# Optimization experiments

Measured on AMD Instinct MI355X. Metric: run time of the kernel, lower is better.

Reference implementation:

```python
import jax, jax.numpy as jnp
import numpy as np

K = 9          # kernel_size
PAD = K // 2   # same padding
SIGMA = 1.0
EPS = 1e-5     # BatchNorm eps


def setup_inputs() -> dict:
    key = jax.random.key(0)
    k0, k1, k2 = jax.random.split(key, 3)
    B, Cin, Cout, L = 4, 64, 64, 131072
    x = jax.random.normal(k0, (B, Cin, L), jnp.float32)
    coords = jax.random.uniform(k1, (B, 3, L), jnp.float32)  # 3D point coords in [0,1)
    W = jax.random.normal(k2, (Cout, Cin, K), jnp.float32) * (1.0 / np.sqrt(Cin * K))
    bias = jnp.zeros((Cout,), jnp.float32)
    gamma = jnp.ones((Cout,), jnp.float32)
    beta = jnp.zeros((Cout,), jnp.float32)
    return {"x": x, "coords": coords, "W": W, "bias": bias, "gamma": gamma, "beta": beta}


def reference(x, coords, W, bias, gamma, beta):
    B, Cin, L = x.shape
    # zero-pad sequence dim for 'same' conv
    xpad = jnp.pad(x, ((0, 0), (0, 0), (PAD, PAD)))
    cpad = jnp.pad(coords, ((0, 0), (0, 0), (PAD, PAD)))
    # unfold: neighbor windows of size K (K is a small compile-time constant)
    x_unf = jnp.stack([xpad[:, :, k:k + L] for k in range(K)], axis=2)   # [B,Cin,K,L]
    c_unf = jnp.stack([cpad[:, :, k:k + L] for k in range(K)], axis=2)   # [B,3,K,L]
    # Gaussian spatial weights from coord distances (WeightedConv1D)
    dist2 = jnp.sum((c_unf - coords[:, :, None, :]) ** 2, axis=1)        # [B,K,L]
    w = jnp.exp(-dist2 / (2.0 * SIGMA * SIGMA))                          # [B,K,L]
    # weighted conv: contract over (Cin, K)
    out = jnp.einsum('ock,bckl->bol', W, x_unf * w[:, None, :, :])       # [B,Cout,L]
    out = out + bias[None, :, None]
    # BatchNorm1d (training-mode batch statistics over B and L) + ReLU
    mean = out.mean(axis=(0, 2), keepdims=True)
    var = out.var(axis=(0, 2), keepdims=True)
    out = (out - mean) * jax.lax.rsqrt(var + EPS)
    out = out * gamma[None, :, None] + beta[None, :, None]
    return jax.nn.relu(out)
```

## Files before the change

kernel.cpp:

```cpp
#include <hip/hip_runtime.h>
#include <hip/hip_bf16.h>

#define KK 9
#define PADK 4
#define CIN 64
#define COUT 64
#define LSEQ 131072
#define NB 4
#define TILEL 128
#define XROWS 136
#define XRS 72
#define NTILES 1024
#define NPART 64
#define TPB 4
#define GRIDC (NB * NTILES / TPB)

typedef __attribute__((ext_vector_type(8))) short v8s;
typedef __attribute__((ext_vector_type(4))) float v4f;

__device__ __forceinline__ unsigned short f2bf(float f) {
  __hip_bfloat16 h = __float2bfloat16(f);
  return *reinterpret_cast<unsigned short*>(&h);
}
__device__ __forceinline__ float bf2f(unsigned short s) {
  return __uint_as_float(((unsigned)s) << 16);
}

__device__ __forceinline__ void store_o(float* p, float v) { *p = v; }
__device__ __forceinline__ void store_o(__hip_bfloat16* p, float v) { *p = __float2bfloat16(v); }

__global__ void wtrans_kernel(const float* __restrict__ W, v8s* __restrict__ Wt) {
  int t = blockIdx.x * 256 + threadIdx.x;
  if (t >= KK * 2 * 4 * 64) return;
  int lane = t & 63;
  int frag = t >> 6;
  int mblk = frag & 3;
  int s    = (frag >> 2) & 1;
  int k    = frag >> 3;
  int m = lane & 15, q = lane >> 4;
  int o = mblk * 16 + m;
  union { v8s v; unsigned short h[8]; } u;
#pragma unroll
  for (int j = 0; j < 8; ++j) {
    int c = 32 * s + q * 8 + j;
    u.h[j] = f2bf(W[(o * CIN + c) * KK + k]);
  }
  Wt[t] = u.v;
}

template <typename OutT>
__global__ __launch_bounds__(256, 3)
void conv_kernel(const float* __restrict__ x, const float* __restrict__ coords,
                 const v8s* __restrict__ Wt, OutT* __restrict__ cv,
                 float* __restrict__ stat_sum, float* __restrict__ stat_sq) {
  __shared__ __align__(16) __hip_bfloat16 xt[2][XROWS][XRS];
  __shared__ float wt[2][KK][TILEL];

  const int tid  = threadIdx.x;
  const int wv   = tid >> 6;
  const int wo   = wv & 1;
  const int wl   = wv >> 1;
  const int lane = tid & 63;
  const int m = lane & 15;
  const int q = lane >> 4;

  const int bid = blockIdx.x;
  const int b   = bid >> 8;
  const int t0  = (bid & 255) * TPB;
  const float* xb = x + (b * CIN) * LSEQ;
  const float* cb = coords + (b * 3) * LSEQ;
  OutT* outb = cv + (b * COUT) * LSEQ;

  const int cg = tid & 7, lc = tid >> 3, c8 = cg * 8;
  const int cn = tid >> 1;
  const int khalf = tid & 1;
  const int k0 = khalf * 4;

  float4 f[8];
  float4 hx;
  float sx, sy, sz;
  float cxk[5], cyk[5], czk[5];

  auto prefetch = [&](int tile) {
    const int l0 = tile * TILEL;
#pragma unroll
    for (int t = 0; t < 8; ++t)
      f[t] = *(const float4*)(xb + (c8 + t) * LSEQ + l0 + 4 * lc);
    if (tid < 128) {
      int side = tid >> 6, c = tid & 63;
      hx = make_float4(0.f, 0.f, 0.f, 0.f);
      if (side == 0) {
        if (tile != 0) hx = *(const float4*)(xb + c * LSEQ + l0 - 4);
      } else {
        if (tile != NTILES - 1) hx = *(const float4*)(xb + c * LSEQ + l0 + TILEL);
      }
    }
    sx = cb[l0 + cn];
    sy = cb[LSEQ + l0 + cn];
    sz = cb[2 * LSEQ + l0 + cn];
#pragma unroll
    for (int i = 0; i < 5; ++i) {
      int l = l0 + cn + (k0 + i) - PADK;
      float cx = 0.f, cy = 0.f, cz = 0.f;
      if ((unsigned)l < (unsigned)LSEQ) {
        cx = cb[l]; cy = cb[LSEQ + l]; cz = cb[2 * LSEQ + l];
      }
      cxk[i] = cx; cyk[i] = cy; czk[i] = cz;
    }
  };

  prefetch(t0);

#pragma unroll 1
  for (int ti = 0; ti < TPB; ++ti) {
    const int tile = t0 + ti;
    const int l0 = tile * TILEL;
    const int cur = ti & 1;

    {
      const float* fp = (const float*)&f[0];
#pragma unroll
      for (int j = 0; j < 4; ++j) {
        union { v8s v; unsigned short h[8]; } u;
#pragma unroll
        for (int t = 0; t < 8; ++t) u.h[t] = f2bf(fp[4 * t + j]);
        *(v8s*)&xt[cur][4 + 4 * lc + j][c8] = u.v;
      }
      if (tid < 128) {
        int side = tid >> 6, c = tid & 63;
        int rb = side ? (TILEL + PADK) : 0;
        xt[cur][rb + 0][c] = __float2bfloat16(hx.x);
        xt[cur][rb + 1][c] = __float2bfloat16(hx.y);
        xt[cur][rb + 2][c] = __float2bfloat16(hx.z);
        xt[cur][rb + 3][c] = __float2bfloat16(hx.w);
      }
      float w5[5];
#pragma unroll
      for (int i = 0; i < 5; ++i) {
        float dx = cxk[i] - sx, dy = cyk[i] - sy, dz = czk[i] - sz;
        w5[i] = __expf(-0.5f * (dx * dx + dy * dy + dz * dz));
      }
      if (khalf == 0) {
#pragma unroll
        for (int i = 0; i < 4; ++i) wt[cur][i][cn] = w5[i] - w5[i + 1];
      } else {
#pragma unroll
        for (int i = 0; i < 4; ++i) wt[cur][4 + i][cn] = w5[i] - w5[i + 1];
        wt[cur][8][cn] = w5[4];
      }
    }

    if (ti + 1 < TPB) prefetch(tile + 1);

    asm volatile("s_waitcnt lgkmcnt(0)" ::: "memory");
    __builtin_amdgcn_s_barrier();

    v4f y[2][4], tot[2][4];
#pragma unroll
    for (int i = 0; i < 2; ++i)
#pragma unroll
      for (int j = 0; j < 4; ++j) {
        y[i][j]   = (v4f){0.f, 0.f, 0.f, 0.f};
        tot[i][j] = (v4f){0.f, 0.f, 0.f, 0.f};
      }

    const v8s* wp = Wt + (wo * 2) * 64 + lane;

#pragma unroll 1
    for (int k = 0; k < KK; ++k) {
#pragma unroll
      for (int s = 0; s < 2; ++s) {
        v8s a0 = wp[k * 512 + s * 256];
        v8s a1 = wp[k * 512 + s * 256 + 64];
#pragma unroll
        for (int nbq = 0; nbq < 4; ++nbq) {
          v8s bf = *(const v8s*)&xt[cur][wl * 64 + nbq * 16 + m + k][q * 8 + 32 * s];
          y[0][nbq] = __builtin_amdgcn_mfma_f32_16x16x32_bf16(a0, bf, y[0][nbq], 0, 0, 0);
          y[1][nbq] = __builtin_amdgcn_mfma_f32_16x16x32_bf16(a1, bf, y[1][nbq], 0, 0, 0);
        }
      }
#pragma unroll
      for (int nbq = 0; nbq < 4; ++nbq) {
        float d = wt[cur][k][wl * 64 + nbq * 16 + m];
#pragma unroll
        for (int mb = 0; mb < 2; ++mb)
#pragma unroll
          for (int r = 0; r < 4; ++r)
            tot[mb][nbq][r] = __builtin_fmaf(d, y[mb][nbq][r], tot[mb][nbq][r]);
      }
    }

    const int part = tile & (NPART - 1);
#pragma unroll
    for (int mb = 0; mb < 2; ++mb) {
#pragma unroll
      for (int r = 0; r < 4; ++r) {
        int o = wo * 32 + mb * 16 + q * 4 + r;
        float s1 = 0.f, s2 = 0.f;
#pragma unroll
        for (int nbq = 0; nbq < 4; ++nbq) {
          float v = tot[mb][nbq][r];
          s1 += v;
          s2 += v * v;
          store_o(&outb[o * LSEQ + l0 + wl * 64 + nbq * 16 + m], v);
        }
#pragma unroll
        for (int off = 1; off < 16; off <<= 1) {
          s1 += __shfl_xor(s1, off, 64);
          s2 += __shfl_xor(s2, off, 64);
        }
        if (m == 0) {
          atomicAdd(&stat_sum[part * COUT + o], s1);
          atomicAdd(&stat_sq [part * COUT + o], s2);
        }
      }
    }
  }
}

__global__ void finalize_kernel(const float* __restrict__ stat_sum,
                                const float* __restrict__ stat_sq,
                                const float* __restrict__ gamma,
                                const float* __restrict__ beta,
                                float* __restrict__ ss) {
  int o = threadIdx.x;
  float s1 = 0.f, s2 = 0.f;
  for (int p = 0; p < NPART; ++p) {
    s1 += stat_sum[p * COUT + o];
    s2 += stat_sq [p * COUT + o];
  }
  const float invN = 1.0f / (float)(NB * LSEQ);
  float mean = s1 * invN;
  float var  = s2 * invN - mean * mean;
  float sc = gamma[o] * rsqrtf(var + 1e-5f);
  ss[o]        = sc;
  ss[COUT + o] = beta[o] - mean * sc;
}

__global__ __launch_bounds__(256)
void scale_f32_kernel(float* __restrict__ data, const float* __restrict__ ss) {
  const int blk = blockIdx.x;
  const int ch = (blk >> 6) & 63;
  const float sc = ss[ch];
  const float sh = ss[COUT + ch];
  const int base = blk * 2048 + threadIdx.x * 8;
  float4 a = *(float4*)(data + base);
  float4 b = *(float4*)(data + base + 4);
  a.x = fmaxf(fmaf(a.x, sc, sh), 0.f);
  a.y = fmaxf(fmaf(a.y, sc, sh), 0.f);
  a.z = fmaxf(fmaf(a.z, sc, sh), 0.f);
  a.w = fmaxf(fmaf(a.w, sc, sh), 0.f);
  b.x = fmaxf(fmaf(b.x, sc, sh), 0.f);
  b.y = fmaxf(fmaf(b.y, sc, sh), 0.f);
  b.z = fmaxf(fmaf(b.z, sc, sh), 0.f);
  b.w = fmaxf(fmaf(b.w, sc, sh), 0.f);
  *(float4*)(data + base)     = a;
  *(float4*)(data + base + 4) = b;
}

__global__ __launch_bounds__(256)
void scale_bf16_kernel(const __hip_bfloat16* __restrict__ cvin,
                       const float* __restrict__ ss, float* __restrict__ out) {
  const int blk = blockIdx.x;
  const int ch = (blk >> 6) & 63;
  const float sc = ss[ch];
  const float sh = ss[COUT + ch];
  const int base = blk * 2048 + threadIdx.x * 8;
  union { v8s v; unsigned short h[8]; } u;
  u.v = *(const v8s*)(cvin + base);
  float r[8];
#pragma unroll
  for (int i = 0; i < 8; ++i)
    r[i] = fmaxf(fmaf(bf2f(u.h[i]), sc, sh), 0.f);
  *(float4*)(out + base)     = make_float4(r[0], r[1], r[2], r[3]);
  *(float4*)(out + base + 4) = make_float4(r[4], r[5], r[6], r[7]);
}

extern "C" void kernel_launch(void* const* d_in, const int* in_sizes, int n_in,
                              void* d_out, int out_size, void* d_ws, size_t ws_size,
                              hipStream_t stream) {
  const float* x      = (const float*)d_in[0];
  const float* coords = (const float*)d_in[1];
  const float* W      = (const float*)d_in[2];
  const float* gamma  = (const float*)d_in[4];
  const float* beta   = (const float*)d_in[5];
  float* out = (float*)d_out;
  char* ws = (char*)d_ws;

  float* stat_sum = (float*)(ws);
  float* stat_sq  = (float*)(ws + 16384);
  float* ss       = (float*)(ws + 32768);
  v8s*   Wt       = (v8s*)(ws + 40960);
  __hip_bfloat16* scratch = (__hip_bfloat16*)(ws + 131072);

  const size_t need_bf16 = (size_t)131072 + (size_t)NB * COUT * LSEQ * 2;
  const bool bf16_path = ws_size >= need_bf16;

  hipMemsetAsync(ws, 0, 32768, stream);
  wtrans_kernel<<<18, 256, 0, stream>>>(W, Wt);

  if (bf16_path) {
    conv_kernel<__hip_bfloat16><<<GRIDC, 256, 0, stream>>>(
        x, coords, Wt, scratch, stat_sum, stat_sq);
    finalize_kernel<<<1, COUT, 0, stream>>>(stat_sum, stat_sq, gamma, beta, ss);
    scale_bf16_kernel<<<(NB * COUT * (LSEQ / 2048)), 256, 0, stream>>>(scratch, ss, out);
  } else {
    conv_kernel<float><<<GRIDC, 256, 0, stream>>>(
        x, coords, Wt, out, stat_sum, stat_sq);
    finalize_kernel<<<1, COUT, 0, stream>>>(stat_sum, stat_sq, gamma, beta, ss);
    scale_f32_kernel<<<(NB * COUT * (LSEQ / 2048)), 256, 0, stream>>>(out, ss);
  }
}
```

Before: 342.5 us.

## Halve conv tile length, raise occupancy, compute weight differences in MFMA loop

Shrinks the sequence tile from 128 to 64 columns, doubling the grid and reducing LDS and register use so five blocks per CU can be resident instead of three. The Gaussian weight differences are now formed inside the K loop from a padded weight row, rather than precomputed. The 16-lane stats shuffle becomes a DPP reduction, and partial sums go into more partitions laid out channel-major so the finalize kernel can read them with vector loads. Smaller tiles mean more halo reloads and more atomics per output element, and the memset covers a larger stats buffer.

Result: slower. 436.2 us (+27.3%).

```diff
diff --git a/kernel.cpp b/kernel.cpp
--- a/kernel.cpp
+++ b/kernel.cpp
@@ -7,15 +7,16 @@
 #define COUT 64
 #define LSEQ 131072
 #define NB 4
-#define TILEL 128
-#define XROWS 136
+#define TILEL 64
+#define XROWS 72
 #define XRS 72
-#define NTILES 1024
-#define NPART 64
+#define NTILES 2048
+#define NPART 256
 #define TPB 4
 #define GRIDC (NB * NTILES / TPB)
 
 typedef __attribute__((ext_vector_type(8))) short v8s;
+typedef __attribute__((ext_vector_type(4))) short v4s;
 typedef __attribute__((ext_vector_type(4))) float v4f;
 
 __device__ __forceinline__ unsigned short f2bf(float f) {
@@ -28,6 +29,19 @@
 
 __device__ __forceinline__ void store_o(float* p, float v) { *p = v; }
 __device__ __forceinline__ void store_o(__hip_bfloat16* p, float v) { *p = __float2bfloat16(v); }
+
+template <int CTRL>
+__device__ __forceinline__ float dppadd(float v) {
+  int s = __builtin_amdgcn_update_dpp(0, __float_as_int(v), CTRL, 0xF, 0xF, true);
+  return v + __int_as_float(s);
+}
+__device__ __forceinline__ float red16(float v) {
+  v = dppadd<0xB1>(v);
+  v = dppadd<0x4E>(v);
+  v = dppadd<0x141>(v);
+  v = dppadd<0x140>(v);
+  return v;
+}
 
 __global__ void wtrans_kernel(const float* __restrict__ W, v8s* __restrict__ Wt) {
   int t = blockIdx.x * 256 + threadIdx.x;
@@ -49,12 +63,12 @@
 }
 
 template <typename OutT>
-__global__ __launch_bounds__(256, 3)
+__global__ __launch_bounds__(256, 5)
 void conv_kernel(const float* __restrict__ x, const float* __restrict__ coords,
                  const v8s* __restrict__ Wt, OutT* __restrict__ cv,
                  float* __restrict__ stat_sum, float* __restrict__ stat_sq) {
   __shared__ __align__(16) __hip_bfloat16 xt[2][XROWS][XRS];
-  __shared__ float wt[2][KK][TILEL];
+  __shared__ float wt[2][KK + 1][TILEL];
 
   const int tid  = threadIdx.x;
   const int wv   = tid >> 6;
@@ -65,27 +79,27 @@
   const int q = lane >> 4;
 
   const int bid = blockIdx.x;
-  const int b   = bid >> 8;
-  const int t0  = (bid & 255) * TPB;
+  const int b   = bid >> 9;
+  const int t0  = (bid & 511) * TPB;
   const float* xb = x + (b * CIN) * LSEQ;
   const float* cb = coords + (b * 3) * LSEQ;
   OutT* outb = cv + (b * COUT) * LSEQ;
 
-  const int cg = tid & 7, lc = tid >> 3, c8 = cg * 8;
-  const int cn = tid >> 1;
-  const int khalf = tid & 1;
-  const int k0 = khalf * 4;
-
-  float4 f[8];
+  const int c4i = tid & 15, c4 = c4i * 4;
+  const int lc  = tid >> 4;
+  const int cn  = tid & 63;
+  const int kq  = tid >> 6;
+
+  float4 f[4];
   float4 hx;
   float sx, sy, sz;
-  float cxk[5], cyk[5], czk[5];
+  float nx[3], ny[3], nz[3];
 
   auto prefetch = [&](int tile) {
     const int l0 = tile * TILEL;
 #pragma unroll
-    for (int t = 0; t < 8; ++t)
-      f[t] = *(const float4*)(xb + (c8 + t) * LSEQ + l0 + 4 * lc);
+    for (int t = 0; t < 4; ++t)
+      f[t] = *(const float4*)(xb + (c4 + t) * LSEQ + l0 + 4 * lc);
     if (tid < 128) {
       int side = tid >> 6, c = tid & 63;
       hx = make_float4(0.f, 0.f, 0.f, 0.f);
@@ -95,17 +109,19 @@
         if (tile != NTILES - 1) hx = *(const float4*)(xb + c * LSEQ + l0 + TILEL);
       }
     }
-    sx = cb[l0 + cn];
-    sy = cb[LSEQ + l0 + cn];
-    sz = cb[2 * LSEQ + l0 + cn];
-#pragma unroll
-    for (int i = 0; i < 5; ++i) {
-      int l = l0 + cn + (k0 + i) - PADK;
-      float cx = 0.f, cy = 0.f, cz = 0.f;
-      if ((unsigned)l < (unsigned)LSEQ) {
-        cx = cb[l]; cy = cb[LSEQ + l]; cz = cb[2 * LSEQ + l];
-      }
-      cxk[i] = cx; cyk[i] = cy; czk[i] = cz;
+    if (kq < 3) {
+      sx = cb[l0 + cn];
+      sy = cb[LSEQ + l0 + cn];
+      sz = cb[2 * LSEQ + l0 + cn];
+#pragma unroll
+      for (int i = 0; i < 3; ++i) {
+        int l = l0 + cn + (kq * 3 + i) - PADK;
+        float cx = 0.f, cy = 0.f, cz = 0.f;
+        if ((unsigned)l < (unsigned)LSEQ) {
+          cx = cb[l]; cy = cb[LSEQ + l]; cz = cb[2 * LSEQ + l];
+        }
+        nx[i] = cx; ny[i] = cy; nz[i] = cz;
+      }
     }
   };
 
@@ -121,10 +137,10 @@
       const float* fp = (const float*)&f[0];
 #pragma unroll
       for (int j = 0; j < 4; ++j) {
-        union { v8s v; unsigned short h[8]; } u;
-#pragma unroll
-        for (int t = 0; t < 8; ++t) u.h[t] = f2bf(fp[4 * t + j]);
-        *(v8s*)&xt[cur][4 + 4 * lc + j][c8] = u.v;
+        union { v4s v; unsigned short h[4]; } u;
+#pragma unroll
+        for (int t = 0; t < 4; ++t) u.h[t] = f2bf(fp[4 * t + j]);
+        *(v4s*)&xt[cur][4 + 4 * lc + j][c4] = u.v;
       }
       if (tid < 128) {
         int side = tid >> 6, c = tid & 63;
@@ -134,19 +150,14 @@
         xt[cur][rb + 2][c] = __float2bfloat16(hx.z);
         xt[cur][rb + 3][c] = __float2bfloat16(hx.w);
       }
-      float w5[5];
-#pragma unroll
-      for (int i = 0; i < 5; ++i) {
-        float dx = cxk[i] - sx, dy = cyk[i] - sy, dz = czk[i] - sz;
-        w5[i] = __expf(-0.5f * (dx * dx + dy * dy + dz * dz));
-      }
-      if (khalf == 0) {
-#pragma unroll
-        for (int i = 0; i < 4; ++i) wt[cur][i][cn] = w5[i] - w5[i + 1];
+      if (kq < 3) {
+#pragma unroll
+        for (int i = 0; i < 3; ++i) {
+          float dx = nx[i] - sx, dy = ny[i] - sy, dz = nz[i] - sz;
+          wt[cur][kq * 3 + i][cn] = __expf(-0.5f * (dx * dx + dy * dy + dz * dz));
+        }
       } else {
-#pragma unroll
-        for (int i = 0; i < 4; ++i) wt[cur][4 + i][cn] = w5[i] - w5[i + 1];
-        wt[cur][8][cn] = w5[4];
+        wt[cur][KK][cn] = 0.f;
       }
     }
 
@@ -155,16 +166,18 @@
     asm volatile("s_waitcnt lgkmcnt(0)" ::: "memory");
     __builtin_amdgcn_s_barrier();
 
-    v4f y[2][4], tot[2][4];
+    v4f y[2][2], tot[2][2];
 #pragma unroll
     for (int i = 0; i < 2; ++i)
 #pragma unroll
-      for (int j = 0; j < 4; ++j) {
+      for (int j = 0; j < 2; ++j) {
         y[i][j]   = (v4f){0.f, 0.f, 0.f, 0.f};
         tot[i][j] = (v4f){0.f, 0.f, 0.f, 0.f};
       }
 
     const v8s* wp = Wt + (wo * 2) * 64 + lane;
+    const int col0 = wl * 32 + m;
+    float wc[2] = { wt[cur][0][col0], wt[cur][0][col0 + 16] };
 
 #pragma unroll 1
     for (int k = 0; k < KK; ++k) {
@@ -173,15 +186,17 @@
         v8s a0 = wp[k * 512 + s * 256];
         v8s a1 = wp[k * 512 + s * 256 + 64];
 #pragma unroll
-        for (int nbq = 0; nbq < 4; ++nbq) {
-          v8s bf = *(const v8s*)&xt[cur][wl * 64 + nbq * 16 + m + k][q * 8 + 32 * s];
+        for (int nbq = 0; nbq < 2; ++nbq) {
+          v8s bf = *(const v8s*)&xt[cur][wl * 32 + nbq * 16 + m + k][q * 8 + 32 * s];
           y[0][nbq] = __builtin_amdgcn_mfma_f32_16x16x32_bf16(a0, bf, y[0][nbq], 0, 0, 0);
           y[1][nbq] = __builtin_amdgcn_mfma_f32_16x16x32_bf16(a1, bf, y[1][nbq], 0, 0, 0);
         }
       }
 #pragma unroll
-      for (int nbq = 0; nbq < 4; ++nbq) {
-        float d = wt[cur][k][wl * 64 + nbq * 16 + m];
+      for (int nbq = 0; nbq < 2; ++nbq) {
+        float wn = wt[cur][k + 1][col0 + nbq * 16];
+        float d = wc[nbq] - wn;
+        wc[nbq] = wn;
 #pragma unroll
         for (int mb = 0; mb < 2; ++mb)
 #pragma unroll
@@ -198,20 +213,17 @@
         int o = wo * 32 + mb * 16 + q * 4 + r;
         float s1 = 0.f, s2 = 0.f;
 #pragma unroll
-        for (int nbq = 0; nbq < 4; ++nbq) {
+        for (int nbq = 0; nbq < 2; ++nbq) {
           float v = tot[mb][nbq][r];
           s1 += v;
           s2 += v * v;
-          store_o(&outb[o * LSEQ + l0 + wl * 64 + nbq * 16 + m], v);
-        }
-#pragma unroll
-        for (int off = 1; off < 16; off <<= 1) {
-          s1 += __shfl_xor(s1, off, 64);
-          s2 += __shfl_xor(s2, off, 64);
-        }
+          store_o(&outb[o * LSEQ + l0 + wl * 32 + nbq * 16 + m], v);
+        }
+        s1 = red16(s1);
+        s2 = red16(s2);
         if (m == 0) {
-          atomicAdd(&stat_sum[part * COUT + o], s1);
-          atomicAdd(&stat_sq [part * COUT + o], s2);
+          atomicAdd(&stat_sum[o * NPART + part], s1);
+          atomicAdd(&stat_sq [o * NPART + part], s2);
         }
       }
     }
@@ -224,10 +236,13 @@
                                 const float* __restrict__ beta,
                                 float* __restrict__ ss) {
   int o = threadIdx.x;
+  const float4* p1 = (const float4*)(stat_sum + o * NPART);
+  const float4* p2 = (const float4*)(stat_sq  + o * NPART);
   float s1 = 0.f, s2 = 0.f;
-  for (int p = 0; p < NPART; ++p) {
-    s1 += stat_sum[p * COUT + o];
-    s2 += stat_sq [p * COUT + o];
+#pragma unroll 4
+  for (int p = 0; p < NPART / 4; ++p) {
+    float4 a = p1[p]; s1 += (a.x + a.y) + (a.z + a.w);
+    float4 c = p2[p]; s2 += (c.x + c.y) + (c.z + c.w);
   }
   const float invN = 1.0f / (float)(NB * LSEQ);
   float mean = s1 * invN;
@@ -288,15 +303,15 @@
   char* ws = (char*)d_ws;
 
   float* stat_sum = (float*)(ws);
-  float* stat_sq  = (float*)(ws + 16384);
-  float* ss       = (float*)(ws + 32768);
-  v8s*   Wt       = (v8s*)(ws + 40960);
-  __hip_bfloat16* scratch = (__hip_bfloat16*)(ws + 131072);
-
-  const size_t need_bf16 = (size_t)131072 + (size_t)NB * COUT * LSEQ * 2;
+  float* stat_sq  = (float*)(ws + 65536);
+  float* ss       = (float*)(ws + 131072);
+  v8s*   Wt       = (v8s*)(ws + 131584);
+  __hip_bfloat16* scratch = (__hip_bfloat16*)(ws + 262144);
+
+  const size_t need_bf16 = (size_t)262144 + (size_t)NB * COUT * LSEQ * 2;
   const bool bf16_path = ws_size >= need_bf16;
 
-  hipMemsetAsync(ws, 0, 32768, stream);
+  hipMemsetAsync(ws, 0, 132096, stream);
   wtrans_kernel<<<18, 256, 0, stream>>>(W, Wt);
 
   if (bf16_path) {
```
